# Optimization experiments

Hardware: AMD Instinct MI355X
Metric: run time of the kernel (lower is better)

## Reference

```python
import jax, jax.numpy as jnp
import numpy as np
from jax import lax

B, S, W = 512, 64, 12        # batch, max words/sentence, chars/word
CV, WV, T = 100, 50000, 45   # char vocab, word vocab, tagset
CE, F, H = 10, 32, 250       # char emb dim, conv filters, lstm hidden
WE = 250                     # word emb dim
IN0 = WE + F                 # lstm layer-0 input = 282


def setup_inputs() -> dict:
    key = jax.random.key(0)
    ks = jax.random.split(key, 16)
    sc = 0.06  # ~1/sqrt(H), keeps LSTM in a sane dynamic range
    return {
        "char_indices": jax.random.randint(ks[0], (B, S, W), 0, CV),
        "word_indices": jax.random.randint(ks[1], (B, S), 0, WV),
        "char_emb": jax.random.normal(ks[2], (CV, CE)) * sc,
        "word_emb": jax.random.normal(ks[3], (WV, WE)) * sc,
        "conv_w": jax.random.normal(ks[4], (F, CE, 3)) * sc,
        "conv_b": jax.random.normal(ks[5], (F,)) * sc,
        "w_ih0": jax.random.normal(ks[6], (4 * H, IN0)) * sc,
        "w_hh0": jax.random.normal(ks[7], (4 * H, H)) * sc,
        "b_ih0": jax.random.normal(ks[8], (4 * H,)) * sc,
        "b_hh0": jax.random.normal(ks[9], (4 * H,)) * sc,
        "w_ih1": jax.random.normal(ks[10], (4 * H, H)) * sc,
        "w_hh1": jax.random.normal(ks[11], (4 * H, H)) * sc,
        "b_ih1": jax.random.normal(ks[12], (4 * H,)) * sc,
        "b_hh1": jax.random.normal(ks[13], (4 * H,)) * sc,
        "dense_w": jax.random.normal(ks[14], (T, H)) * sc,
        "dense_b": jax.random.normal(ks[15], (T,)) * sc,
    }


def lstm_layer(x_seq, w_ih, w_hh, b_ih, b_hh):
    """x_seq: (S, B, IN). PyTorch gate order i,f,g,o. Zero initial state."""
    h0 = jnp.zeros((B, H), x_seq.dtype)
    c0 = jnp.zeros((B, H), x_seq.dtype)
    # precompute input projections for all steps: (S, B, 4H)
    xg = jnp.einsum('sbi,gi->sbg', x_seq, w_ih) + b_ih + b_hh

    def step(carry, xg_t):
        h, c = carry
        gates = xg_t + h @ w_hh.T
        i, f, g, o = jnp.split(gates, 4, axis=-1)
        c = jax.nn.sigmoid(f) * c + jax.nn.sigmoid(i) * jnp.tanh(g)
        h = jax.nn.sigmoid(o) * jnp.tanh(c)
        return (h, c), h

    _, hs = lax.scan(step, (h0, c0), xg)
    return hs  # (S, B, H)


def reference(char_indices, word_indices, char_emb, word_emb, conv_w, conv_b,
              w_ih0, w_hh0, b_ih0, b_hh0, w_ih1, w_hh1, b_ih1, b_hh1,
              dense_w, dense_b):
    # char-level word embeddings: embed -> conv1d(k=3, pad=1) -> max over chars
    ce = char_emb[char_indices]                       # (B, S, W, CE)
    x = ce.reshape(B * S, W, CE).transpose(0, 2, 1)   # (B*S, CE, W)
    y = lax.conv_general_dilated(x, conv_w, (1,), [(1, 1)],
                                 dimension_numbers=('NCH', 'OIH', 'NCH'))
    y = y + conv_b[None, :, None]                     # (B*S, F, W)
    char_word = y.max(axis=2).reshape(B, S, F)        # (B, S, F)

    we = word_emb[word_indices]                       # (B, S, WE)
    emb = jnp.concatenate([char_word, we], axis=-1)   # (B, S, F+WE)

    # NOTE: original uses .view(S, B, -1) (a reshape, NOT a transpose);
    # we replicate that exact data layout for faithfulness.
    x_seq = emb.reshape(S, B, IN0)

    h1 = lstm_layer(x_seq, w_ih0, w_hh0, b_ih0, b_hh0)  # (S, B, H)
    h2 = lstm_layer(h1, w_ih1, w_hh1, b_ih1, b_hh1)     # (S, B, H)

    # again a raw .view(B, S, -1) reshape in the original
    out = h2.reshape(B, S, H)
    tag_space = out @ dense_w.T + dense_b               # (B, S, T)
    return tag_space
```

## Files before the change

### kernel.cpp

```cpp
#include <hip/hip_runtime.h>
#include <hip/hip_bf16.h>


#define Bb 512
#define Ss 64
#define Ww 12
#define Tt 45
#define CEe 10
#define Ff 32
#define Hh 250
#define Mtok (Bb*Ss)
#define KP0 288
#define KP1 256
#define NGP 1024
#define XPAD 1036
#define NB 4
#define NBLK (Bb/NB)
#define NRES 7

typedef float f32x4 __attribute__((ext_vector_type(4)));
typedef __bf16 bf16x8 __attribute__((ext_vector_type(8)));

__device__ inline unsigned short f2bu(float f) {
  return __builtin_bit_cast(unsigned short, __float2bfloat16(f));
}
__device__ inline float bu2f(unsigned short u) {
  return __bfloat162float(__builtin_bit_cast(__hip_bfloat16, u));
}
__device__ inline float sigm(float x) { return 1.f / (1.f + __expf(-x)); }
__device__ inline float tanh_f(float x) { float e = __expf(2.f*x); return 1.f - 2.f/(e+1.f); }

__device__ inline float ldf(const void* p, size_t i, int f32) {
  return f32 ? ((const float*)p)[i] : bu2f(((const unsigned short*)p)[i]);
}
__device__ inline unsigned short ldb(const void* p, size_t i, int f32) {
  return f32 ? f2bu(((const float*)p)[i]) : ((const unsigned short*)p)[i];
}

__global__ void detect_dtype(const unsigned short* __restrict__ wemb_u16, int* __restrict__ flag) {
  if (threadIdx.x == 0) {
    int cnt = 0;
    for (int i = 0; i < 64; ++i) {
      unsigned short v = wemb_u16[2*i];
      int e = (v >> 7) & 0xFF;
      cnt += (e >= 127) ? 1 : 0;
    }
    *flag = (cnt > 0) ? 1 : 0;
  }
}

#define R_WIH0 (1024*288)
#define R_W256 (1024*256)
#define R_WD   (128*256)
#define PREP_TOTAL (R_WIH0 + 3*R_W256 + R_WD + 1024 + 1024 + 128)

__global__ void prep_weights(const void* __restrict__ wih0, const void* __restrict__ wih1,
                             const void* __restrict__ whh0, const void* __restrict__ whh1,
                             const void* __restrict__ dw,
                             const void* __restrict__ bih0, const void* __restrict__ bhh0,
                             const void* __restrict__ bih1, const void* __restrict__ bhh1,
                             const void* __restrict__ db,
                             unsigned short* __restrict__ wih0p, unsigned short* __restrict__ wih1p,
                             unsigned short* __restrict__ whh0p, unsigned short* __restrict__ whh1p,
                             unsigned short* __restrict__ wdp,
                             float* __restrict__ bias0, float* __restrict__ bias1, float* __restrict__ biasd,
                             const int* __restrict__ flagp)
{
  const int f = *flagp;
  int idx = blockIdx.x * 256 + threadIdx.x;
  if (idx < R_WIH0) {
    int n = idx / 288, k = idx % 288;
    wih0p[idx] = (n < 1000 && k < 282) ? ldb(wih0, (size_t)n*282 + k, f) : 0;
    return;
  }
  idx -= R_WIH0;
  if (idx < R_W256) { int n = idx/256, k = idx%256; wih1p[idx] = (n<1000 && k<250) ? ldb(wih1, (size_t)n*250+k, f) : 0; return; }
  idx -= R_W256;
  if (idx < R_W256) {
    int e = idx & 7, lane = (idx>>3)&63, kt = (idx>>9)&7, t = (idx>>12)&1, g = (idx>>13)&3, w = idx>>15;
    int r = lane & 15, q = lane >> 4;
    int jj = w*32 + t*16 + r, k = kt*32 + q*8 + e;
    whh0p[idx] = (jj<250 && k<250) ? ldb(whh0, (size_t)(g*250+jj)*250 + k, f) : 0;
    return;
  }
  idx -= R_W256;
  if (idx < R_W256) {
    int e = idx & 7, lane = (idx>>3)&63, kt = (idx>>9)&7, t = (idx>>12)&1, g = (idx>>13)&3, w = idx>>15;
    int r = lane & 15, q = lane >> 4;
    int jj = w*32 + t*16 + r, k = kt*32 + q*8 + e;
    whh1p[idx] = (jj<250 && k<250) ? ldb(whh1, (size_t)(g*250+jj)*250 + k, f) : 0;
    return;
  }
  idx -= R_W256;
  if (idx < R_WD)   { int n = idx/256, k = idx%256; wdp[idx] = (n<45 && k<250) ? ldb(dw, (size_t)n*250+k, f) : 0; return; }
  idx -= R_WD;
  if (idx < 1024) { bias0[idx] = (idx<1000) ? ldf(bih0, idx, f) + ldf(bhh0, idx, f) : 0.f; return; }
  idx -= 1024;
  if (idx < 1024) { bias1[idx] = (idx<1000) ? ldf(bih1, idx, f) + ldf(bhh1, idx, f) : 0.f; return; }
  idx -= 1024;
  if (idx < 128)  { biasd[idx] = (idx<45) ? ldf(db, idx, f) : 0.f; }
}

__global__ void embed_conv(const int* __restrict__ ci, const int* __restrict__ wi,
                           const void* __restrict__ cemb,
                           const void* __restrict__ wemb,
                           const void* __restrict__ cw,
                           const void* __restrict__ cb,
                           unsigned short* __restrict__ emb,
                           const int* __restrict__ flagp)
{
  __shared__ float s_cw[960];
  __shared__ float s_cb[32];
  __shared__ float s_ce[1000];
  __shared__ int   s_ind[4][12];
  __shared__ float s_ct[4][120];
  const int f = *flagp;
  const int tid = threadIdx.x;
  for (int i = tid; i < 960; i += 256) s_cw[i] = ldf(cw, i, f);
  if (tid < 32) s_cb[tid] = ldf(cb, tid, f);
  for (int i = tid; i < 1000; i += 256) s_ce[i] = ldf(cemb, i, f);
  __syncthreads();
  const int wv = tid >> 6, lane = tid & 63;
  const int tok = blockIdx.x * 4 + wv;
  if (lane < 12) s_ind[wv][lane] = ci[tok*12 + lane];
  __syncthreads();
#pragma unroll
  for (int p = 0; p < 2; ++p) {
    int pos = p*64 + lane;
    if (pos < 120) {
      int w = pos / 10, ce = pos % 10;
      s_ct[wv][pos] = s_ce[s_ind[wv][w]*10 + ce];
    }
  }
  __syncthreads();
  if (lane < 32) {
    const int ff = lane;
    float mx = -1e30f;
    for (int p = 0; p < Ww; ++p) {
      float acc = s_cb[ff];
#pragma unroll
      for (int k = 0; k < 3; ++k) {
        int wp = p + k - 1;
        if (wp >= 0 && wp < Ww) {
#pragma unroll
          for (int ce = 0; ce < CEe; ++ce)
            acc += s_ct[wv][wp*10 + ce] * s_cw[ff*30 + ce*3 + k];
        }
      }
      mx = fmaxf(mx, acc);
    }
    emb[(size_t)tok*KP0 + ff] = f2bu(mx);
  }
  const int widx = wi[tok];
  for (int j = lane; j < 250; j += 64)
    emb[(size_t)tok*KP0 + Ff + j] = ldb(wemb, (size_t)widx*250 + j, f);
  if (lane >= 58) emb[(size_t)tok*KP0 + 282 + (lane - 58)] = 0;
}

template<int KC>
__global__ __launch_bounds__(256, 2) void gemm_bf16(
    const unsigned short* __restrict__ A, int lda,
    const unsigned short* __restrict__ Bw,
    const float* __restrict__ bias,
    void* __restrict__ Cout, int ldo, int nvalid,
    const int* __restrict__ flagp, int useflag, int gate_pad)
{
  __shared__ alignas(16) unsigned short lsA[128*32];
  __shared__ alignas(16) unsigned short lsB[128*32];
  const int tid = threadIdx.x;
  const int lane = tid & 63;
  const int w = tid >> 6;
  const int wr = w >> 1, wc = w & 1;
  const int mt = blockIdx.x, nt = blockIdx.y;

  f32x4 acc[4][4];
#pragma unroll
  for (int m = 0; m < 4; ++m)
#pragma unroll
    for (int n = 0; n < 4; ++n) acc[m][n] = (f32x4){0.f,0.f,0.f,0.f};

  for (int kt = 0; kt < KC; ++kt) {
    __syncthreads();
#pragma unroll
    for (int p = 0; p < 2; ++p) {
      int flat = p*256 + tid;
      int row = flat >> 2, c = flat & 3;
      *(bf16x8*)&lsA[flat*8] = *(const bf16x8*)(A  + (size_t)(mt*128 + row)*lda     + kt*32 + c*8);
      *(bf16x8*)&lsB[flat*8] = *(const bf16x8*)(Bw + (size_t)(nt*128 + row)*(KC*32) + kt*32 + c*8);
    }
    __syncthreads();
    bf16x8 a[4], b[4];
#pragma unroll
    for (int m = 0; m < 4; ++m) {
      int row = wr*64 + m*16 + (lane & 15);
      a[m] = *(const bf16x8*)&lsA[row*32 + (lane >> 4)*8];
    }
#pragma unroll
    for (int n = 0; n < 4; ++n) {
      int row = wc*64 + n*16 + (lane & 15);
      b[n] = *(const bf16x8*)&lsB[row*32 + (lane >> 4)*8];
    }
#pragma unroll
    for (int m = 0; m < 4; ++m)
#pragma unroll
      for (int n = 0; n < 4; ++n)
        acc[m][n] = __builtin_amdgcn_mfma_f32_16x16x32_bf16(a[m], b[n], acc[m][n], 0, 0, 0);
  }

  const bool of32 = useflag && (*flagp != 0);
  const int rbase = mt*128 + wr*64;
  const int cbase = nt*128 + wc*64;
#pragma unroll
  for (int m = 0; m < 4; ++m)
#pragma unroll
    for (int n = 0; n < 4; ++n) {
      int col = cbase + n*16 + (lane & 15);
      if (col < nvalid) {
        float bv = bias[col];
        int colw = col;
        if (gate_pad) {
          int g = (col>=250) + (col>=500) + (col>=750);
          colw = col + 6*g;
        }
#pragma unroll
        for (int j = 0; j < 4; ++j) {
          int row = rbase + m*16 + (lane >> 4)*4 + j;
          float val = acc[m][n][j] + bv;
          if (of32) ((float*)Cout)[(size_t)row*ldo + colw] = val;
          else      ((unsigned short*)Cout)[(size_t)row*ldo + colw] = f2bu(val);
        }
      }
    }
}

__global__ __launch_bounds__(1024) void lstm_c(
    const unsigned short* __restrict__ xg,
    const unsigned short* __restrict__ whh,
    unsigned short* __restrict__ hout)
{
  __shared__ alignas(16) unsigned short whl[16*NRES*64*8];
  __shared__ alignas(16) unsigned short h_s[16*256];
  __shared__ alignas(16) unsigned short xg_l[2][NB*XPAD];
  __shared__ float g_s[NB][1028];
  __shared__ float c_s[NB][260];
  const int tid = threadIdx.x;
  const int lane = tid & 63;
  const int w = tid >> 6;
  const int r = lane & 15, q = lane >> 4;
  const int bb0 = blockIdx.x * NB;
  const unsigned short* wbase = whh + (size_t)(w >> 1)*32768 + (size_t)(w & 1)*4096 + lane*8;

#pragma unroll
  for (int f = 0; f < NRES; ++f)
    *(bf16x8*)&whl[((w*NRES + f)*64 + lane)*8] = *(const bf16x8*)(wbase + f*512);

  for (int i = tid; i < 16*256; i += 1024) h_s[i] = 0;
  for (int i = tid; i < NB*260; i += 1024) ((float*)c_s)[i] = 0.f;
  if (tid < NB*128) {
    int row = tid >> 7, ch = tid & 127;
    *(bf16x8*)&xg_l[0][row*XPAD + ch*8] =
        *(const bf16x8*)(xg + (size_t)(bb0 + row)*1024 + ch*8);
  }
  __syncthreads();

  int cur = 0;
#pragma unroll 1
  for (int s = 0; s < Ss; ++s) {
    const int sp = (s + 1 < Ss) ? s + 1 : s;
    bf16x8 pf;
    if (tid < NB*128) {
      int row = tid >> 7, ch = tid & 127;
      pf = *(const bf16x8*)(xg + (size_t)(sp*512 + bb0 + row)*1024 + ch*8);
    }
    bf16x8 av[8];
#pragma unroll
    for (int kt = 0; kt < 8; ++kt) {
      int ch = (kt*4 + q) ^ (r & 7);
      av[kt] = *(const bf16x8*)&h_s[r*256 + ch*8];
    }
    {
      f32x4 a = (f32x4){0.f,0.f,0.f,0.f};
#pragma unroll
      for (int kt = 0; kt < NRES; ++kt) {
        bf16x8 bv = *(const bf16x8*)&whl[((w*NRES + kt)*64 + lane)*8];
        a = __builtin_amdgcn_mfma_f32_16x16x32_bf16(av[kt], bv, a, 0, 0, 0);
      }
      {
        bf16x8 bv = *(const bf16x8*)(wbase + 7*512);
        a = __builtin_amdgcn_mfma_f32_16x16x32_bf16(av[7], bv, a, 0, 0, 0);
      }
      if (q == 0) {
        const int gcol = (w << 4) + r;
#pragma unroll
        for (int j = 0; j < 4; ++j) g_s[j][gcol] = a[j];
      }
    }
#pragma unroll 1
    for (int g = 1; g < 4; ++g) {
      const unsigned short* bp = wbase + g*8192;
      f32x4 a = (f32x4){0.f,0.f,0.f,0.f};
#pragma unroll
      for (int kt = 0; kt < 8; ++kt) {
        bf16x8 bv = *(const bf16x8*)(bp + kt*512);
        a = __builtin_amdgcn_mfma_f32_16x16x32_bf16(av[kt], bv, a, 0, 0, 0);
      }
      if (q == 0) {
        const int gcol = g*256 + (w << 4) + r;
#pragma unroll
        for (int j = 0; j < 4; ++j) g_s[j][gcol] = a[j];
      }
    }
    __syncthreads();
    {
      const unsigned short* xc = &xg_l[cur][0];
      const int b = tid >> 8, j = tid & 255;
      float gi = g_s[b][j]       + bu2f(xc[b*XPAD + j]);
      float gf = g_s[b][256 + j] + bu2f(xc[b*XPAD + 256 + j]);
      float gg = g_s[b][512 + j] + bu2f(xc[b*XPAD + 512 + j]);
      float go = g_s[b][768 + j] + bu2f(xc[b*XPAD + 768 + j]);
      float c = sigm(gf)*c_s[b][j] + sigm(gi)*tanh_f(gg);
      float h = sigm(go)*tanh_f(c);
      if (j >= Hh) { c = 0.f; h = 0.f; }
      c_s[b][j] = c;
      unsigned short hb = f2bu(h);
      h_s[b*256 + (((j >> 3) ^ (b & 7)) << 3) + (j & 7)] = hb;
      hout[(size_t)(s*512 + bb0 + b)*256 + j] = hb;
    }
    if (tid < NB*128) {
      int row = tid >> 7, ch = tid & 127;
      *(bf16x8*)&xg_l[cur ^ 1][row*XPAD + ch*8] = pf;
    }
    __syncthreads();
    cur ^= 1;
  }
}

extern "C" void kernel_launch(void* const* d_in, const int* in_sizes, int n_in,
                              void* d_out, int out_size, void* d_ws, size_t ws_size,
                              hipStream_t stream) {
  (void)in_sizes; (void)n_in; (void)out_size;
  const int* ci = (const int*)d_in[0];
  const int* wi = (const int*)d_in[1];
  const void* cemb = d_in[2];
  const void* wemb = d_in[3];
  const void* cw   = d_in[4];
  const void* cb   = d_in[5];
  const void* wih0 = d_in[6];
  const void* whh0 = d_in[7];
  const void* bih0 = d_in[8];
  const void* bhh0 = d_in[9];
  const void* wih1 = d_in[10];
  const void* whh1 = d_in[11];
  const void* bih1 = d_in[12];
  const void* bhh1 = d_in[13];
  const void* dw   = d_in[14];
  const void* db   = d_in[15];

  constexpr size_t OFF_WIH0 = 0;
  constexpr size_t OFF_WIH1 = OFF_WIH0 + 589824;
  constexpr size_t OFF_WHH0 = OFF_WIH1 + 524288;
  constexpr size_t OFF_WHH1 = OFF_WHH0 + 524288;
  constexpr size_t OFF_WD   = OFF_WHH1 + 524288;
  constexpr size_t OFF_B0   = OFF_WD   + 65536;
  constexpr size_t OFF_B1   = OFF_B0   + 4096;
  constexpr size_t OFF_BD   = OFF_B1   + 4096;
  constexpr size_t OFF_FLAG = OFF_BD   + 2048;
  constexpr size_t OFF_H1   = OFF_BD   + 4096;
  constexpr size_t OFF_EMB  = OFF_H1   + 16777216;
  constexpr size_t OFF_XG   = OFF_EMB  + 18874368;
  constexpr size_t WS_NEED  = OFF_XG   + 67108864;
  if (ws_size < WS_NEED) return;

  char* ws = (char*)d_ws;
  unsigned short* WIH0 = (unsigned short*)(ws + OFF_WIH0);
  unsigned short* WIH1 = (unsigned short*)(ws + OFF_WIH1);
  unsigned short* WHH0 = (unsigned short*)(ws + OFF_WHH0);
  unsigned short* WHH1 = (unsigned short*)(ws + OFF_WHH1);
  unsigned short* WD   = (unsigned short*)(ws + OFF_WD);
  float* B0 = (float*)(ws + OFF_B0);
  float* B1 = (float*)(ws + OFF_B1);
  float* BD = (float*)(ws + OFF_BD);
  int* FLAG = (int*)(ws + OFF_FLAG);
  unsigned short* H1   = (unsigned short*)(ws + OFF_H1);
  unsigned short* EMB  = (unsigned short*)(ws + OFF_EMB);
  unsigned short* H2   = (unsigned short*)(ws + OFF_EMB);
  unsigned short* XG   = (unsigned short*)(ws + OFF_XG);

  detect_dtype<<<1, 64, 0, stream>>>((const unsigned short*)wemb, FLAG);
  prep_weights<<<(PREP_TOTAL + 255)/256, 256, 0, stream>>>(
      wih0, wih1, whh0, whh1, dw, bih0, bhh0, bih1, bhh1, db,
      WIH0, WIH1, WHH0, WHH1, WD, B0, B1, BD, FLAG);
  embed_conv<<<Mtok/4, 256, 0, stream>>>(ci, wi, cemb, wemb, cw, cb, EMB, FLAG);
  gemm_bf16<9><<<dim3(Mtok/128, NGP/128), 256, 0, stream>>>(EMB, KP0, WIH0, B0, XG, NGP, NGP, FLAG, 0, 1);
  lstm_c<<<NBLK, 1024, 0, stream>>>(XG, WHH0, H1);
  gemm_bf16<8><<<dim3(Mtok/128, NGP/128), 256, 0, stream>>>(H1, KP1, WIH1, B1, XG, NGP, NGP, FLAG, 0, 1);
  lstm_c<<<NBLK, 1024, 0, stream>>>(XG, WHH1, H2);
  gemm_bf16<8><<<dim3(Mtok/128, 1), 256, 0, stream>>>(H2, KP1, WD, BD, d_out, Tt, Tt, FLAG, 1, 0);
}
```

Before: 669.1 us.

## Fuse LSTM gate math into MFMA lanes and double-buffer hidden state

Each wave now keeps all four gate accumulators in registers and computes the cell update directly in the q==0 lanes, so the gate-staging shared array and one barrier per step go away. The cell state moves into registers, and the hidden state is double-buffered by step parity so the next step's reads do not race with the current writes. The trade-off is that only 16 of 64 lanes run the elementwise work, four rows each, and register pressure rises from the four live accumulators and the fully unrolled gate loop.

```diff
diff --git a/kernel.cpp b/kernel.cpp
--- a/kernel.cpp
+++ b/kernel.cpp
@@ -239,23 +239,24 @@
     unsigned short* __restrict__ hout)
 {
   __shared__ alignas(16) unsigned short whl[16*NRES*64*8];
-  __shared__ alignas(16) unsigned short h_s[16*256];
+  __shared__ alignas(16) unsigned short h_s[2][16*256];
   __shared__ alignas(16) unsigned short xg_l[2][NB*XPAD];
-  __shared__ float g_s[NB][1028];
-  __shared__ float c_s[NB][260];
   const int tid = threadIdx.x;
   const int lane = tid & 63;
   const int w = tid >> 6;
   const int r = lane & 15, q = lane >> 4;
   const int bb0 = blockIdx.x * NB;
   const unsigned short* wbase = whh + (size_t)(w >> 1)*32768 + (size_t)(w & 1)*4096 + lane*8;
+  const int col = w*16 + r;
 
 #pragma unroll
   for (int f = 0; f < NRES; ++f)
     *(bf16x8*)&whl[((w*NRES + f)*64 + lane)*8] = *(const bf16x8*)(wbase + f*512);
 
-  for (int i = tid; i < 16*256; i += 1024) h_s[i] = 0;
-  for (int i = tid; i < NB*260; i += 1024) ((float*)c_s)[i] = 0.f;
+  for (int i = tid; i < 2*16*256; i += 1024) ((unsigned short*)h_s)[i] = 0;
+  float c_reg[4];
+#pragma unroll
+  for (int j = 0; j < 4; ++j) c_reg[j] = 0.f;
   if (tid < NB*128) {
     int row = tid >> 7, ch = tid & 127;
     *(bf16x8*)&xg_l[0][row*XPAD + ch*8] =
@@ -266,6 +267,7 @@
   int cur = 0;
 #pragma unroll 1
   for (int s = 0; s < Ss; ++s) {
+    const int par = s & 1;
     const int sp = (s + 1 < Ss) ? s + 1 : s;
     bf16x8 pf;
     if (tid < NB*128) {
@@ -276,55 +278,46 @@
 #pragma unroll
     for (int kt = 0; kt < 8; ++kt) {
       int ch = (kt*4 + q) ^ (r & 7);
-      av[kt] = *(const bf16x8*)&h_s[r*256 + ch*8];
+      av[kt] = *(const bf16x8*)&h_s[par][r*256 + ch*8];
+    }
+    f32x4 acc[4];
+#pragma unroll
+    for (int g = 0; g < 4; ++g) acc[g] = (f32x4){0.f,0.f,0.f,0.f};
+#pragma unroll
+    for (int kt = 0; kt < NRES; ++kt) {
+      bf16x8 bv = *(const bf16x8*)&whl[((w*NRES + kt)*64 + lane)*8];
+      acc[0] = __builtin_amdgcn_mfma_f32_16x16x32_bf16(av[kt], bv, acc[0], 0, 0, 0);
     }
     {
-      f32x4 a = (f32x4){0.f,0.f,0.f,0.f};
-#pragma unroll
-      for (int kt = 0; kt < NRES; ++kt) {
-        bf16x8 bv = *(const bf16x8*)&whl[((w*NRES + kt)*64 + lane)*8];
-        a = __builtin_amdgcn_mfma_f32_16x16x32_bf16(av[kt], bv, a, 0, 0, 0);
-      }
-      {
-        bf16x8 bv = *(const bf16x8*)(wbase + 7*512);
-        a = __builtin_amdgcn_mfma_f32_16x16x32_bf16(av[7], bv, a, 0, 0, 0);
-      }
-      if (q == 0) {
-        const int gcol = (w << 4) + r;
-#pragma unroll
-        for (int j = 0; j < 4; ++j) g_s[j][gcol] = a[j];
-      }
-    }
-#pragma unroll 1
+      bf16x8 bv = *(const bf16x8*)(wbase + 7*512);
+      acc[0] = __builtin_amdgcn_mfma_f32_16x16x32_bf16(av[7], bv, acc[0], 0, 0, 0);
+    }
+#pragma unroll
     for (int g = 1; g < 4; ++g) {
       const unsigned short* bp = wbase + g*8192;
-      f32x4 a = (f32x4){0.f,0.f,0.f,0.f};
 #pragma unroll
       for (int kt = 0; kt < 8; ++kt) {
-        bf16x8 bv = *(const bf16x8*)(bp + kt*512);
-        a = __builtin_amdgcn_mfma_f32_16x16x32_bf16(av[kt], bv, a, 0, 0, 0);
+        bf16x8 bv = *(const bf16x8*)(bp + kt*32*16);
+        acc[g] = __builtin_amdgcn_mfma_f32_16x16x32_bf16(av[kt], bv, acc[g], 0, 0, 0);
       }
-      if (q == 0) {
-        const int gcol = g*256 + (w << 4) + r;
-#pragma unroll
-        for (int j = 0; j < 4; ++j) g_s[j][gcol] = a[j];
+    }
+    if (q == 0) {
+      const unsigned short* xc = &xg_l[cur][0];
+      const bool valid = col < Hh;
+#pragma unroll
+      for (int j = 0; j < 4; ++j) {
+        float gi = acc[0][j] + bu2f(xc[j*XPAD + col]);
+        float gf = acc[1][j] + bu2f(xc[j*XPAD + 256 + col]);
+        float gg = acc[2][j] + bu2f(xc[j*XPAD + 512 + col]);
+        float go = acc[3][j] + bu2f(xc[j*XPAD + 768 + col]);
+        float c = sigm(gf)*c_reg[j] + sigm(gi)*tanh_f(gg);
+        float h = sigm(go)*tanh_f(c);
+        if (!valid) { c = 0.f; h = 0.f; }
+        c_reg[j] = c;
+        unsigned short hb = f2bu(h);
+        h_s[par ^ 1][j*256 + (((col >> 3) ^ (j & 7)) << 3) + (col & 7)] = hb;
+        hout[(size_t)(s*512 + bb0 + j)*256 + col] = hb;
       }
-    }
-    __syncthreads();
-    {
-      const unsigned short* xc = &xg_l[cur][0];
-      const int b = tid >> 8, j = tid & 255;
-      float gi = g_s[b][j]       + bu2f(xc[b*XPAD + j]);
-      float gf = g_s[b][256 + j] + bu2f(xc[b*XPAD + 256 + j]);
-      float gg = g_s[b][512 + j] + bu2f(xc[b*XPAD + 512 + j]);
-      float go = g_s[b][768 + j] + bu2f(xc[b*XPAD + 768 + j]);
-      float c = sigm(gf)*c_s[b][j] + sigm(gi)*tanh_f(gg);
-      float h = sigm(go)*tanh_f(c);
-      if (j >= Hh) { c = 0.f; h = 0.f; }
-      c_s[b][j] = c;
-      unsigned short hb = f2bu(h);
-      h_s[b*256 + (((j >> 3) ^ (b & 7)) << 3) + (j & 7)] = hb;
-      hout[(size_t)(s*512 + bb0 + b)*256 + j] = hb;
     }
     if (tid < NB*128) {
       int row = tid >> 7, ch = tid & 127;
```

Result: slower. 1.005 ms (+50.2%).
